# Optimization experiments

Measured on AMD Instinct MI355X. Metric: run time of the kernel, lower is better.

Reference implementation:

```python
import jax, jax.numpy as jnp
import numpy as np

D_MODEL = 1024
N_HEADS = 16
D_HEAD = 64
NUM_REL_POS = 2047
B = 8
L = 1024


def setup_inputs() -> dict:
    key = jax.random.key(0)
    ks = jax.random.split(key, 8)
    s = 1.0 / np.sqrt(D_MODEL)
    x = jax.random.normal(ks[0], (B, L, D_MODEL), dtype=jnp.float32)
    rel_indices = jax.random.randint(ks[1], (L, L), 0, NUM_REL_POS)
    Wq = jax.random.normal(ks[2], (D_MODEL, D_MODEL), dtype=jnp.float32) * s
    Wk = jax.random.normal(ks[3], (D_MODEL, D_MODEL), dtype=jnp.float32) * s
    Wv = jax.random.normal(ks[4], (D_MODEL, D_MODEL), dtype=jnp.float32) * s
    Wo = jax.random.normal(ks[5], (D_MODEL, D_MODEL), dtype=jnp.float32) * s
    rel_k = jax.random.normal(ks[6], (NUM_REL_POS, D_HEAD), dtype=jnp.float32) * 0.02
    rel_v = jax.random.normal(ks[7], (NUM_REL_POS, D_HEAD), dtype=jnp.float32) * 0.02
    return {"x": x, "rel_indices": rel_indices, "Wq": Wq, "Wk": Wk,
            "Wv": Wv, "Wo": Wo, "rel_k": rel_k, "rel_v": rel_v}


def reference(x, rel_indices, Wq, Wk, Wv, Wo, rel_k, rel_v):
    Bz, Ls, D = x.shape
    H, dk = N_HEADS, D_HEAD
    scale = 1.0 / np.sqrt(dk)
    # torch Linear: y = x @ W.T, weights are [out, in]
    q = jnp.einsum('bld,ed->ble', x, Wq).reshape(Bz, Ls, H, dk).transpose(0, 2, 1, 3)
    k = jnp.einsum('bld,ed->ble', x, Wk).reshape(Bz, Ls, H, dk).transpose(0, 2, 1, 3)
    v = jnp.einsum('bld,ed->ble', x, Wv).reshape(Bz, Ls, H, dk).transpose(0, 2, 1, 3)
    r_k = rel_k[rel_indices]  # (L, L, dk)
    r_v = rel_v[rel_indices]  # (L, L, dk)
    content = jnp.einsum('bhid,bhjd->bhij', q, k)
    rel = jnp.einsum('bhid,ijd->bhij', q, r_k)
    scores = (content + rel) * scale
    probs = jax.nn.softmax(scores, axis=-1)  # dropout = 0 (eval)
    out = jnp.einsum('bhij,bhjd->bhid', probs, v) + jnp.einsum('bhij,ijd->bhid', probs, r_v)
    out = out.transpose(0, 2, 1, 3).reshape(Bz, Ls, D)
    return jnp.einsum('bld,ed->ble', out, Wo)
```

## Files before the change

kernel.cpp:

```cpp
#include <hip/hip_runtime.h>

#define B_ 8
#define H_ 16
#define L_ 1024
#define DH_ 64
#define DM_ 1024
#define NP_ 2047
#define NP2_ 2048
#define SCALE_ 0.125f

#define PS_ 1032
#define HS_ 516

typedef __attribute__((ext_vector_type(8))) short bf16x8;
typedef __attribute__((ext_vector_type(4))) float f32x4;

__device__ __forceinline__ unsigned short f2bf(float x) {
    union { float f; unsigned int u; } v; v.f = x;
    return (unsigned short)((v.u + 0x7FFFu + ((v.u >> 16) & 1u)) >> 16);
}
__device__ __forceinline__ float bf2f(unsigned short b) {
    union { unsigned int u; float f; } v; v.u = ((unsigned int)b) << 16;
    return v.f;
}

template <int MODE>
__global__ __launch_bounds__(256) void proj_gemm(const float* __restrict__ X,
                                                 const float* __restrict__ W,
                                                 float* __restrict__ Yf,
                                                 unsigned short* __restrict__ Y0,
                                                 unsigned short* __restrict__ Y1)
{
    __shared__ __align__(16) float As[16][68];
    __shared__ __align__(16) float Bs[16][68];
    const int t   = threadIdx.x;
    const int tm  = t & 15;
    const int tn  = t >> 4;
    const int row0 = blockIdx.x * 64;
    const int col0 = blockIdx.y * 64;
    const int lr = t >> 2;
    const int lc = (t & 3) * 4;

    float acc[4][4];
#pragma unroll
    for (int i = 0; i < 4; ++i)
#pragma unroll
        for (int j = 0; j < 4; ++j) acc[i][j] = 0.f;

    for (int k0 = 0; k0 < DM_; k0 += 16) {
        float4 av = *(const float4*)(X + (size_t)(row0 + lr) * DM_ + k0 + lc);
        float4 wv = *(const float4*)(W + (size_t)(col0 + lr) * DM_ + k0 + lc);
        __syncthreads();
        As[lc + 0][lr] = av.x; As[lc + 1][lr] = av.y;
        As[lc + 2][lr] = av.z; As[lc + 3][lr] = av.w;
        Bs[lc + 0][lr] = wv.x; Bs[lc + 1][lr] = wv.y;
        Bs[lc + 2][lr] = wv.z; Bs[lc + 3][lr] = wv.w;
        __syncthreads();
#pragma unroll
        for (int kk = 0; kk < 16; ++kk) {
            float4 a  = *(const float4*)&As[kk][tm * 4];
            float4 w4 = *(const float4*)&Bs[kk][tn * 4];
            acc[0][0] = fmaf(a.x, w4.x, acc[0][0]);
            acc[0][1] = fmaf(a.x, w4.y, acc[0][1]);
            acc[0][2] = fmaf(a.x, w4.z, acc[0][2]);
            acc[0][3] = fmaf(a.x, w4.w, acc[0][3]);
            acc[1][0] = fmaf(a.y, w4.x, acc[1][0]);
            acc[1][1] = fmaf(a.y, w4.y, acc[1][1]);
            acc[1][2] = fmaf(a.y, w4.z, acc[1][2]);
            acc[1][3] = fmaf(a.y, w4.w, acc[1][3]);
            acc[2][0] = fmaf(a.z, w4.x, acc[2][0]);
            acc[2][1] = fmaf(a.z, w4.y, acc[2][1]);
            acc[2][2] = fmaf(a.z, w4.z, acc[2][2]);
            acc[2][3] = fmaf(a.z, w4.w, acc[2][3]);
            acc[3][0] = fmaf(a.w, w4.x, acc[3][0]);
            acc[3][1] = fmaf(a.w, w4.y, acc[3][1]);
            acc[3][2] = fmaf(a.w, w4.z, acc[3][2]);
            acc[3][3] = fmaf(a.w, w4.w, acc[3][3]);
        }
    }

    const int h = blockIdx.y;
#pragma unroll
    for (int i = 0; i < 4; ++i) {
        const int row = row0 + tm * 4 + i;
        if (MODE == 1) {
            float4 r = make_float4(acc[i][0], acc[i][1], acc[i][2], acc[i][3]);
            *(float4*)(Yf + (size_t)row * DM_ + col0 + tn * 4) = r;
        } else {
            const int bb = row >> 10;
            const int l  = row & 1023;
            if (MODE == 0) {
                ushort4 hi4, lo4;
                unsigned short* hp = (unsigned short*)&hi4;
                unsigned short* lp = (unsigned short*)&lo4;
#pragma unroll
                for (int j = 0; j < 4; ++j) {
                    unsigned short hb = f2bf(acc[i][j]);
                    hp[j] = hb;
                    lp[j] = f2bf(acc[i][j] - bf2f(hb));
                }
                const size_t base = (((size_t)bb * H_ + h) * L_ + l) * DH_ + tn * 4;
                *(ushort4*)(Y0 + base) = hi4;
                *(ushort4*)(Y1 + base) = lo4;
            } else {
#pragma unroll
                for (int j = 0; j < 4; ++j) {
                    const int d = tn * 4 + j;
                    Y0[(((size_t)bb * H_ + h) * DH_ + d) * L_ + l] = f2bf(acc[i][j]);
                }
            }
        }
    }
}

__global__ __launch_bounds__(256) void prep_rel(const float* __restrict__ rk,
                                                const float* __restrict__ rv,
                                                unsigned short* __restrict__ rk_hi,
                                                unsigned short* __restrict__ rv_t)
{
    const int idx = blockIdx.x * 256 + threadIdx.x;
    const int p = idx >> 6;
    const int d = idx & 63;
    float xk = (p < NP_) ? rk[(size_t)p * DH_ + d] : 0.f;
    rk_hi[idx] = f2bf(xk);
    float xv = (p < NP_) ? rv[(size_t)p * DH_ + d] : 0.f;
    rv_t[(size_t)d * NP2_ + p] = f2bf(xv);
}

__global__ __launch_bounds__(512, 4) void shaw_attn_mfma(
    const unsigned short* __restrict__ qh, const unsigned short* __restrict__ ql,
    const unsigned short* __restrict__ kh, const unsigned short* __restrict__ kl,
    const unsigned short* __restrict__ vt, const int* __restrict__ ridx,
    const unsigned short* __restrict__ rkh, const unsigned short* __restrict__ rvt,
    float* __restrict__ out)
{
    __shared__ __align__(16) unsigned char regionA[16 * PS_ * 2];
    __shared__ __align__(16) unsigned char regionB[16 * HS_ * 4];
    __shared__ float pmax[16][8];
    __shared__ float psum[16][8];

    char*           qrel8 = (char*)regionA;
    unsigned short* Pu    = (unsigned short*)regionA;
    float*          hist  = (float*)regionB;
    float*          red   = (float*)regionB;

    const int t    = threadIdx.x;
    const int w    = t >> 6;
    const int lane = t & 63;
    const int mrow = lane & 15;
    const int grp  = lane >> 4;
    const int i0   = blockIdx.x * 16;
    const int h    = blockIdx.y;
    const int b    = blockIdx.z;
    const size_t bh = (size_t)b * H_ + h;

    const unsigned short* qhp = qh + bh * (size_t)(L_ * DH_);
    const unsigned short* qlp = ql + bh * (size_t)(L_ * DH_);
    const unsigned short* khp = kh + bh * (size_t)(L_ * DH_);
    const unsigned short* klp = kl + bh * (size_t)(L_ * DH_);
    const unsigned short* vtp = vt + bh * (size_t)(DH_ * L_);

    bf16x8 qAh[2], qAl[2];
#pragma unroll
    for (int s = 0; s < 2; ++s) {
        const size_t off = (size_t)(i0 + mrow) * DH_ + s * 32 + grp * 8;
        qAh[s] = *(const bf16x8*)(qhp + off);
        qAl[s] = *(const bf16x8*)(qlp + off);
    }

#pragma unroll 4
    for (int tt = 0; tt < 16; ++tt) {
        const int pcol = (w * 16 + tt) * 16 + mrow;
        const size_t boff = (size_t)pcol * DH_ + grp * 8;
        bf16x8 Bh0 = *(const bf16x8*)(rkh + boff);
        bf16x8 Bh1 = *(const bf16x8*)(rkh + boff + 32);
        f32x4 c = {0.f, 0.f, 0.f, 0.f};
        c = __builtin_amdgcn_mfma_f32_16x16x32_bf16(qAh[0], Bh0, c, 0, 0, 0);
        c = __builtin_amdgcn_mfma_f32_16x16x32_bf16(qAh[1], Bh1, c, 0, 0, 0);
        unsigned int pk = 0;
#pragma unroll
        for (int r = 0; r < 4; ++r) {
            int qi = (int)rintf(c[r] * 128.f);
            qi = qi > 127 ? 127 : (qi < -127 ? -127 : qi);
            pk |= ((unsigned int)(qi & 0xff)) << (8 * r);
        }
        *(unsigned int*)(qrel8 + pcol * 16 + grp * 4) = pk;
    }
    __syncthreads();

    float sc[8][4];
#pragma unroll 2
    for (int tt = 0; tt < 8; ++tt) {
        const int jcol = (w * 8 + tt) * 16 + mrow;
        const size_t boff = (size_t)jcol * DH_ + grp * 8;
        bf16x8 Bh0 = *(const bf16x8*)(khp + boff);
        bf16x8 Bh1 = *(const bf16x8*)(khp + boff + 32);
        bf16x8 Bl0 = *(const bf16x8*)(klp + boff);
        bf16x8 Bl1 = *(const bf16x8*)(klp + boff + 32);
        f32x4 c = {0.f, 0.f, 0.f, 0.f};
        c = __builtin_amdgcn_mfma_f32_16x16x32_bf16(qAh[0], Bh0, c, 0, 0, 0);
        c = __builtin_amdgcn_mfma_f32_16x16x32_bf16(qAh[1], Bh1, c, 0, 0, 0);
        c = __builtin_amdgcn_mfma_f32_16x16x32_bf16(qAh[0], Bl0, c, 0, 0, 0);
        c = __builtin_amdgcn_mfma_f32_16x16x32_bf16(qAh[1], Bl1, c, 0, 0, 0);
        c = __builtin_amdgcn_mfma_f32_16x16x32_bf16(qAl[0], Bh0, c, 0, 0, 0);
        c = __builtin_amdgcn_mfma_f32_16x16x32_bf16(qAl[1], Bh1, c, 0, 0, 0);
#pragma unroll
        for (int r = 0; r < 4; ++r) {
            const int rr = grp * 4 + r;
            const int pidx = ridx[(size_t)(i0 + rr) * L_ + jcol];
            const float rel = (float)qrel8[pidx * 16 + grp * 4 + r];
            sc[tt][r] = fmaf(rel, SCALE_ / 128.f, c[r] * SCALE_);
        }
    }

    float mx[4];
#pragma unroll
    for (int r = 0; r < 4; ++r) {
        float m = sc[0][r];
#pragma unroll
        for (int tt = 1; tt < 8; ++tt) m = fmaxf(m, sc[tt][r]);
#pragma unroll
        for (int off = 1; off < 16; off <<= 1) m = fmaxf(m, __shfl_xor(m, off));
        mx[r] = m;
    }
    {
        const float wv0 = (mrow == 0) ? mx[0] : (mrow == 1) ? mx[1] : (mrow == 2) ? mx[2] : mx[3];
        if (mrow < 4) pmax[grp * 4 + mrow][w] = wv0;
    }
    __syncthreads();

    float gm[4];
#pragma unroll
    for (int r = 0; r < 4; ++r) {
        const int rr = grp * 4 + r;
        float m = pmax[rr][0];
#pragma unroll
        for (int u = 1; u < 8; ++u) m = fmaxf(m, pmax[rr][u]);
        gm[r] = m;
    }
    float sm[4];
#pragma unroll
    for (int r = 0; r < 4; ++r) {
        const int rr = grp * 4 + r;
        float s = 0.f;
#pragma unroll
        for (int tt = 0; tt < 8; ++tt) {
            const float e = __expf(sc[tt][r] - gm[r]);
            s += e;
            Pu[rr * PS_ + (w * 8 + tt) * 16 + mrow] = f2bf(e);
        }
#pragma unroll
        for (int off = 1; off < 16; off <<= 1) s += __shfl_xor(s, off);
        sm[r] = s;
    }
    {
        const float sv0 = (mrow == 0) ? sm[0] : (mrow == 1) ? sm[1] : (mrow == 2) ? sm[2] : sm[3];
        if (mrow < 4) psum[grp * 4 + mrow][w] = sv0;
    }
    __syncthreads();

    const int n = w & 3;
    const int khalf = w >> 2;
    f32x4 acc = {0.f, 0.f, 0.f, 0.f};
    {
        const unsigned short* vcol = vtp + (size_t)(n * 16 + mrow) * L_;
#pragma unroll 4
        for (int s = 0; s < 16; ++s) {
            const int kb = khalf * 512 + s * 32;
            bf16x8 a = *(const bf16x8*)(Pu + mrow * PS_ + kb + grp * 8);
            bf16x8 bb = *(const bf16x8*)(vcol + kb + grp * 8);
            acc = __builtin_amdgcn_mfma_f32_16x16x32_bf16(a, bb, acc, 0, 0, 0);
        }
    }

    unsigned int cache[32];
    {
        const int* idx0 = ridx + (size_t)(i0 + 2 * w) * L_;
        const int* idx1 = idx0 + L_;
#pragma unroll
        for (int c = 0; c < 16; ++c) {
            const int j = c * 64 + lane;
            cache[c]      = (((unsigned int)idx0[j]) << 16) | (unsigned int)Pu[(2 * w) * PS_ + j];
            cache[c + 16] = (((unsigned int)idx1[j]) << 16) | (unsigned int)Pu[(2 * w + 1) * PS_ + j];
        }
    }

    for (int pass = 0; pass < 4; ++pass) {
        __syncthreads();
        for (int z = t; z < 16 * HS_; z += 512) hist[z] = 0.f;
        __syncthreads();
#pragma unroll
        for (int e = 0; e < 32; ++e) {
            const unsigned int pk = cache[e];
            const int pidx = (int)(pk >> 16);
            if ((pidx >> 9) == pass) {
                const int row = 2 * w + (e >> 4);
                atomicAdd(&hist[row * HS_ + (pidx & 511)], bf2f((unsigned short)(pk & 0xffffu)));
            }
        }
        __syncthreads();
        const unsigned short* rvcol = rvt + (size_t)(n * 16 + mrow) * NP2_ + pass * 512;
#pragma unroll
        for (int s = 0; s < 8; ++s) {
            const int kb = khalf * 256 + s * 32;
            const f32x4* hp = (const f32x4*)&hist[mrow * HS_ + kb + grp * 8];
            f32x4 h0 = hp[0], h1 = hp[1];
            bf16x8 a;
#pragma unroll
            for (int e = 0; e < 4; ++e) { a[e] = (short)f2bf(h0[e]); a[e + 4] = (short)f2bf(h1[e]); }
            bf16x8 bb = *(const bf16x8*)(rvcol + kb + grp * 8);
            acc = __builtin_amdgcn_mfma_f32_16x16x32_bf16(a, bb, acc, 0, 0, 0);
        }
    }

    __syncthreads();
#pragma unroll
    for (int r = 0; r < 4; ++r) red[w * 320 + (grp * 4 + r) * 20 + mrow] = acc[r];
    __syncthreads();
    if (w < 4) {
#pragma unroll
        for (int r = 0; r < 4; ++r) {
            const int rr = grp * 4 + r;
            float o = red[w * 320 + rr * 20 + mrow] + red[(w + 4) * 320 + rr * 20 + mrow];
            float ssum = 0.f;
#pragma unroll
            for (int u = 0; u < 8; ++u) ssum += psum[rr][u];
            out[((size_t)b * L_ + i0 + rr) * DM_ + h * DH_ + w * 16 + mrow] = o / ssum;
        }
    }
}

extern "C" void kernel_launch(void* const* d_in, const int* in_sizes, int n_in,
                              void* d_out, int out_size, void* d_ws, size_t ws_size,
                              hipStream_t stream)
{
    const float* x    = (const float*)d_in[0];
    const int*   ridx = (const int*)  d_in[1];
    const float* Wq   = (const float*)d_in[2];
    const float* Wk   = (const float*)d_in[3];
    const float* Wv   = (const float*)d_in[4];
    const float* Wo   = (const float*)d_in[5];
    const float* rk   = (const float*)d_in[6];
    const float* rv   = (const float*)d_in[7];
    float* out = (float*)d_out;

    const size_t NQ = (size_t)B_ * H_ * L_ * DH_;
    float* attn = (float*)d_ws;
    unsigned short* u = (unsigned short*)(attn + NQ);
    unsigned short* qh = u;            u += NQ;
    unsigned short* ql = u;            u += NQ;
    unsigned short* kh = u;            u += NQ;
    unsigned short* kl = u;            u += NQ;
    unsigned short* vt = u;            u += NQ;
    unsigned short* rkh = u;           u += (size_t)NP2_ * DH_;
    unsigned short* rvt = u;           u += (size_t)NP2_ * DH_;

    dim3 gthr(256);
    dim3 ggrid((B_ * L_) / 64, DM_ / 64);

    prep_rel<<<dim3((NP2_ * DH_) / 256), gthr, 0, stream>>>(rk, rv, rkh, rvt);
    proj_gemm<0><<<ggrid, gthr, 0, stream>>>(x, Wq, nullptr, qh, ql);
    proj_gemm<0><<<ggrid, gthr, 0, stream>>>(x, Wk, nullptr, kh, kl);
    proj_gemm<2><<<ggrid, gthr, 0, stream>>>(x, Wv, nullptr, vt, nullptr);

    shaw_attn_mfma<<<dim3(L_ / 16, H_, B_), dim3(512), 0, stream>>>(
        qh, ql, kh, kl, vt, ridx, rkh, rvt, attn);

    proj_gemm<1><<<ggrid, gthr, 0, stream>>>(attn, Wo, out, nullptr, nullptr);
}
```

Measured before the change: 2.405 ms.

## Remap attention blocks across XCDs, unroll loads, prefetch rel_v and index gathers

Launches the attention kernel on a 1D grid and remaps block IDs so consecutive blocks on each of the 8 XCDs share the same (batch, head), improving L2 reuse of K/V. Fully unrolls the rel-K, QK and PV loops, batches the rel-index gathers separately from the MFMAs, prefetches rel_v fragments before the histogram barriers, and vectorizes the histogram clear. It also drops the min-waves-per-EU launch bound, which lets the compiler use more registers at the risk of lower occupancy.

```diff
diff --git a/kernel.cpp b/kernel.cpp
--- a/kernel.cpp
+++ b/kernel.cpp
@@ -127,7 +127,7 @@
     rv_t[(size_t)d * NP2_ + p] = f2bf(xv);
 }
 
-__global__ __launch_bounds__(512, 4) void shaw_attn_mfma(
+__global__ __launch_bounds__(512) void shaw_attn_mfma(
     const unsigned short* __restrict__ qh, const unsigned short* __restrict__ ql,
     const unsigned short* __restrict__ kh, const unsigned short* __restrict__ kl,
     const unsigned short* __restrict__ vt, const int* __restrict__ ridx,
@@ -149,9 +149,12 @@
     const int lane = t & 63;
     const int mrow = lane & 15;
     const int grp  = lane >> 4;
-    const int i0   = blockIdx.x * 16;
-    const int h    = blockIdx.y;
-    const int b    = blockIdx.z;
+
+    const int bid = blockIdx.x;
+    const int lid = (bid & 7) * 1024 + (bid >> 3);
+    const int b   = lid >> 10;
+    const int h   = (lid >> 6) & 15;
+    const int i0  = (lid & 63) * 16;
     const size_t bh = (size_t)b * H_ + h;
 
     const unsigned short* qhp = qh + bh * (size_t)(L_ * DH_);
@@ -168,49 +171,66 @@
         qAl[s] = *(const bf16x8*)(qlp + off);
     }
 
-#pragma unroll 4
-    for (int tt = 0; tt < 16; ++tt) {
-        const int pcol = (w * 16 + tt) * 16 + mrow;
-        const size_t boff = (size_t)pcol * DH_ + grp * 8;
-        bf16x8 Bh0 = *(const bf16x8*)(rkh + boff);
-        bf16x8 Bh1 = *(const bf16x8*)(rkh + boff + 32);
-        f32x4 c = {0.f, 0.f, 0.f, 0.f};
-        c = __builtin_amdgcn_mfma_f32_16x16x32_bf16(qAh[0], Bh0, c, 0, 0, 0);
-        c = __builtin_amdgcn_mfma_f32_16x16x32_bf16(qAh[1], Bh1, c, 0, 0, 0);
-        unsigned int pk = 0;
-#pragma unroll
-        for (int r = 0; r < 4; ++r) {
-            int qi = (int)rintf(c[r] * 128.f);
-            qi = qi > 127 ? 127 : (qi < -127 ? -127 : qi);
-            pk |= ((unsigned int)(qi & 0xff)) << (8 * r);
-        }
-        *(unsigned int*)(qrel8 + pcol * 16 + grp * 4) = pk;
+    {
+        const unsigned short* rb = rkh + (size_t)(w * 256 + mrow) * DH_ + grp * 8;
+#pragma unroll
+        for (int tt = 0; tt < 16; ++tt) {
+            bf16x8 Bh0 = *(const bf16x8*)(rb + tt * 1024);
+            bf16x8 Bh1 = *(const bf16x8*)(rb + tt * 1024 + 32);
+            f32x4 c = {0.f, 0.f, 0.f, 0.f};
+            c = __builtin_amdgcn_mfma_f32_16x16x32_bf16(qAh[0], Bh0, c, 0, 0, 0);
+            c = __builtin_amdgcn_mfma_f32_16x16x32_bf16(qAh[1], Bh1, c, 0, 0, 0);
+            const int pcol = (w * 16 + tt) * 16 + mrow;
+            unsigned int pk = 0;
+#pragma unroll
+            for (int r = 0; r < 4; ++r) {
+                int qi = (int)rintf(c[r] * 128.f);
+                qi = qi > 127 ? 127 : (qi < -127 ? -127 : qi);
+                pk |= ((unsigned int)(qi & 0xff)) << (8 * r);
+            }
+            *(unsigned int*)(qrel8 + pcol * 16 + grp * 4) = pk;
+        }
     }
     __syncthreads();
 
     float sc[8][4];
-#pragma unroll 2
-    for (int tt = 0; tt < 8; ++tt) {
-        const int jcol = (w * 8 + tt) * 16 + mrow;
-        const size_t boff = (size_t)jcol * DH_ + grp * 8;
-        bf16x8 Bh0 = *(const bf16x8*)(khp + boff);
-        bf16x8 Bh1 = *(const bf16x8*)(khp + boff + 32);
-        bf16x8 Bl0 = *(const bf16x8*)(klp + boff);
-        bf16x8 Bl1 = *(const bf16x8*)(klp + boff + 32);
-        f32x4 c = {0.f, 0.f, 0.f, 0.f};
-        c = __builtin_amdgcn_mfma_f32_16x16x32_bf16(qAh[0], Bh0, c, 0, 0, 0);
-        c = __builtin_amdgcn_mfma_f32_16x16x32_bf16(qAh[1], Bh1, c, 0, 0, 0);
-        c = __builtin_amdgcn_mfma_f32_16x16x32_bf16(qAh[0], Bl0, c, 0, 0, 0);
-        c = __builtin_amdgcn_mfma_f32_16x16x32_bf16(qAh[1], Bl1, c, 0, 0, 0);
-        c = __builtin_amdgcn_mfma_f32_16x16x32_bf16(qAl[0], Bh0, c, 0, 0, 0);
-        c = __builtin_amdgcn_mfma_f32_16x16x32_bf16(qAl[1], Bh1, c, 0, 0, 0);
-#pragma unroll
-        for (int r = 0; r < 4; ++r) {
-            const int rr = grp * 4 + r;
-            const int pidx = ridx[(size_t)(i0 + rr) * L_ + jcol];
-            const float rel = (float)qrel8[pidx * 16 + grp * 4 + r];
-            sc[tt][r] = fmaf(rel, SCALE_ / 128.f, c[r] * SCALE_);
-        }
+    {
+        const unsigned short* kbh = khp + (size_t)(w * 128 + mrow) * DH_ + grp * 8;
+        const unsigned short* kbl = klp + (size_t)(w * 128 + mrow) * DH_ + grp * 8;
+#pragma unroll
+        for (int tt = 0; tt < 8; ++tt) {
+            bf16x8 Bh0 = *(const bf16x8*)(kbh + tt * 1024);
+            bf16x8 Bh1 = *(const bf16x8*)(kbh + tt * 1024 + 32);
+            bf16x8 Bl0 = *(const bf16x8*)(kbl + tt * 1024);
+            bf16x8 Bl1 = *(const bf16x8*)(kbl + tt * 1024 + 32);
+            f32x4 c = {0.f, 0.f, 0.f, 0.f};
+            c = __builtin_amdgcn_mfma_f32_16x16x32_bf16(qAh[0], Bh0, c, 0, 0, 0);
+            c = __builtin_amdgcn_mfma_f32_16x16x32_bf16(qAh[1], Bh1, c, 0, 0, 0);
+            c = __builtin_amdgcn_mfma_f32_16x16x32_bf16(qAh[0], Bl0, c, 0, 0, 0);
+            c = __builtin_amdgcn_mfma_f32_16x16x32_bf16(qAh[1], Bl1, c, 0, 0, 0);
+            c = __builtin_amdgcn_mfma_f32_16x16x32_bf16(qAl[0], Bh0, c, 0, 0, 0);
+            c = __builtin_amdgcn_mfma_f32_16x16x32_bf16(qAl[1], Bh1, c, 0, 0, 0);
+#pragma unroll
+            for (int r = 0; r < 4; ++r) sc[tt][r] = c[r] * SCALE_;
+        }
+    }
+
+    {
+        int pidxA[8][4];
+#pragma unroll
+        for (int tt = 0; tt < 8; ++tt) {
+            const int jcol = (w * 8 + tt) * 16 + mrow;
+#pragma unroll
+            for (int r = 0; r < 4; ++r)
+                pidxA[tt][r] = ridx[(size_t)(i0 + grp * 4 + r) * L_ + jcol];
+        }
+#pragma unroll
+        for (int tt = 0; tt < 8; ++tt)
+#pragma unroll
+            for (int r = 0; r < 4; ++r) {
+                const float rel = (float)qrel8[pidxA[tt][r] * 16 + grp * 4 + r];
+                sc[tt][r] = fmaf(rel, SCALE_ / 128.f, sc[tt][r]);
+            }
     }
 
     float mx[4];
@@ -263,12 +283,11 @@
     const int khalf = w >> 2;
     f32x4 acc = {0.f, 0.f, 0.f, 0.f};
     {
-        const unsigned short* vcol = vtp + (size_t)(n * 16 + mrow) * L_;
-#pragma unroll 4
+        const unsigned short* vcol = vtp + (size_t)(n * 16 + mrow) * L_ + khalf * 512 + grp * 8;
+#pragma unroll
         for (int s = 0; s < 16; ++s) {
-            const int kb = khalf * 512 + s * 32;
-            bf16x8 a = *(const bf16x8*)(Pu + mrow * PS_ + kb + grp * 8);
-            bf16x8 bb = *(const bf16x8*)(vcol + kb + grp * 8);
+            bf16x8 a  = *(const bf16x8*)(Pu + mrow * PS_ + khalf * 512 + s * 32 + grp * 8);
+            bf16x8 bb = *(const bf16x8*)(vcol + s * 32);
             acc = __builtin_amdgcn_mfma_f32_16x16x32_bf16(a, bb, acc, 0, 0, 0);
         }
     }
@@ -286,8 +305,19 @@
     }
 
     for (int pass = 0; pass < 4; ++pass) {
-        __syncthreads();
-        for (int z = t; z < 16 * HS_; z += 512) hist[z] = 0.f;
+        bf16x8 rvf[8];
+        {
+            const unsigned short* rvcol =
+                rvt + (size_t)(n * 16 + mrow) * NP2_ + pass * 512 + khalf * 256 + grp * 8;
+#pragma unroll
+            for (int s = 0; s < 8; ++s) rvf[s] = *(const bf16x8*)(rvcol + s * 32);
+        }
+        __syncthreads();
+        {
+            float4* h4 = (float4*)hist;
+            const float4 z4 = make_float4(0.f, 0.f, 0.f, 0.f);
+            for (int z = t; z < (16 * HS_) / 4; z += 512) h4[z] = z4;
+        }
         __syncthreads();
 #pragma unroll
         for (int e = 0; e < 32; ++e) {
@@ -299,7 +329,6 @@
             }
         }
         __syncthreads();
-        const unsigned short* rvcol = rvt + (size_t)(n * 16 + mrow) * NP2_ + pass * 512;
 #pragma unroll
         for (int s = 0; s < 8; ++s) {
             const int kb = khalf * 256 + s * 32;
@@ -308,8 +337,7 @@
             bf16x8 a;
 #pragma unroll
             for (int e = 0; e < 4; ++e) { a[e] = (short)f2bf(h0[e]); a[e + 4] = (short)f2bf(h1[e]); }
-            bf16x8 bb = *(const bf16x8*)(rvcol + kb + grp * 8);
-            acc = __builtin_amdgcn_mfma_f32_16x16x32_bf16(a, bb, acc, 0, 0, 0);
+            acc = __builtin_amdgcn_mfma_f32_16x16x32_bf16(a, rvf[s], acc, 0, 0, 0);
         }
     }
 
@@ -363,7 +391,7 @@
     proj_gemm<0><<<ggrid, gthr, 0, stream>>>(x, Wk, nullptr, kh, kl);
     proj_gemm<2><<<ggrid, gthr, 0, stream>>>(x, Wv, nullptr, vt, nullptr);
 
-    shaw_attn_mfma<<<dim3(L_ / 16, H_, B_), dim3(512), 0, stream>>>(
+    shaw_attn_mfma<<<dim3(8192), dim3(512), 0, stream>>>(
         qh, ql, kh, kl, vt, ridx, rkh, rvt, attn);
 
     proj_gemm<1><<<ggrid, gthr, 0, stream>>>(attn, Wo, out, nullptr, nullptr);
```

Measured after the change: 2.551 ms. 6.1% more time.
